# Kernel tuning notes

Measured on AMD Instinct MI355X. Metric: run time of the kernel, lower is better.

The kernel has to match this reference:

```python
import jax, jax.numpy as jnp
import numpy as np

EPS = 1e-12
B, DIN, T, DH = 32, 512, 4096, 500


def setup_inputs() -> dict:
    key = jax.random.key(0)
    k1, k2, k3 = jax.random.split(key, 3)
    x = jax.random.normal(k1, (B, DIN, T), dtype=jnp.float32)
    weight1 = jax.random.normal(k2, (DH, DIN), dtype=jnp.float32) * (1.0 / np.sqrt(DIN))
    weight2 = jax.random.normal(k3, (1, DH), dtype=jnp.float32) * (1.0 / np.sqrt(DH))
    return {"x": x, "weight1": weight1, "weight2": weight2, "dim": 2}


def reference(x, weight1, weight2, dim):
    # x: (B, din, T)
    h = jnp.swapaxes(x, 1, 2)                      # (B, T, din)
    a = jax.nn.relu(jnp.einsum('btd,hd->bth', h, weight1))  # (B, T, dh)
    scores = jnp.einsum('bth,oh->bto', a, weight2)           # (B, T, 1)
    attn = jax.nn.softmax(scores, axis=1)                    # softmax over time
    mean = jnp.einsum('bdt,bto->bdo', x, attn)               # (B, din, 1)
    variance = jnp.mean((x - mean) ** 2, axis=dim)           # (B, din) unweighted
    mean_s = jnp.squeeze(mean, axis=dim)                     # (B, din)
    mask = (variance <= EPS).astype(variance.dtype)
    variance = (1.0 - mask) * variance + mask * EPS
    stddev = jnp.sqrt(variance)
    return jnp.concatenate((mean_s, stddev), axis=-1)        # (B, 2*din)
```

## Files before the change

kernel.cpp:

```cpp
#include <hip/hip_runtime.h>
#include <hip/hip_bf16.h>

#define NB 32
#define DIN 512
#define TT 4096
#define DH 500
#define DHP 512
#define EPSV 1e-12f
#define BM 128
#define LDA 520
#define NTILES (TT / BM)
#define CHD 128
#define NCHK 4

typedef short short8 __attribute__((ext_vector_type(8)));
typedef float f32x16 __attribute__((ext_vector_type(16)));

__device__ inline unsigned short f2bf(float f) {
    unsigned int u = __builtin_bit_cast(unsigned int, f);
    unsigned int r = (u + 0x7fffu + ((u >> 16) & 1u)) >> 16;
    return (unsigned short)r;
}
__device__ inline float bf2f(unsigned short h) {
    unsigned int u = ((unsigned int)h) << 16;
    return __builtin_bit_cast(float, u);
}

__global__ void prep_kernel(const float* __restrict__ w1, const float* __restrict__ w2,
                            unsigned short* __restrict__ w1b, float* __restrict__ w2f) {
    int idx = blockIdx.x * blockDim.x + threadIdx.x;
    if (idx < DHP * DIN) {
        const int j    = idx & 7;
        const int lane = (idx >> 3) & 63;
        const int ks   = (idx >> 9) & 31;
        const int hb   = idx >> 14;
        const int h = hb * 32 + (lane & 31);
        const int d = ks * 16 + (lane >> 5) * 8 + j;
        float v = (h < DH) ? w1[h * DIN + d] : 0.f;
        w1b[idx] = f2bf(v);
        if (idx < DHP) w2f[idx] = (idx < DH) ? w2[idx] : 0.f;
    }
}

__launch_bounds__(512, 2)
__global__ void scores_fused(const float* __restrict__ x,
                             const unsigned short* __restrict__ w1b,
                             const float* __restrict__ w2f,
                             float* __restrict__ pm, float* __restrict__ pz,
                             float* __restrict__ pswx, float* __restrict__ psx,
                             float* __restrict__ psx2) {
    __shared__ unsigned short A_lds[BM][LDA];
    __shared__ float score_p[8][BM];
    __shared__ float w_lds[BM];
    __shared__ float red[4];

    const int tid = threadIdx.x;
    const int b  = blockIdx.x >> 5;
    const int t0 = (blockIdx.x & 31) * BM;

    const int tsub  = tid & 63;
    const int thalf = (tid >> 6) & 1;
    const int ts    = thalf * 64 + tsub;
    const int dg    = tid >> 7;
    const float* xb = x + (size_t)b * DIN * TT + t0 + ts;

    const int w = tid >> 6;
    const int lane = tid & 63;
    const int lane31 = lane & 31;
    const int khalf = lane >> 5;
    const int hrow0 = w * 64;
    const unsigned short* base0 = w1b + (size_t)w * 32768 + (size_t)lane * 8;
    const unsigned short* base1 = base0 + 16384;

    {
        float xr[32];
        #pragma unroll
        for (int j = 0; j < 32; ++j)
            xr[j] = xb[(size_t)(dg * 32 + j) * TT];
        #pragma unroll
        for (int oct = 0; oct < 4; ++oct) {
            short8 pk;
            #pragma unroll
            for (int j = 0; j < 8; ++j) pk[j] = (short)f2bf(xr[oct * 8 + j]);
            *reinterpret_cast<short8*>(&A_lds[ts][dg * 32 + oct * 8]) = pk;
        }
    }
    __syncthreads();

    f32x16 acc[2][4];
    #pragma unroll
    for (int p = 0; p < 2; ++p)
        #pragma unroll
        for (int tt = 0; tt < 4; ++tt)
            #pragma unroll
            for (int g = 0; g < 16; ++g) acc[p][tt][g] = 0.f;

    #pragma unroll
    for (int c = 0; c < NCHK; ++c) {
        float xr[32];
        if (c < NCHK - 1) {
            const int db = (c + 1) * CHD + dg * 32;
            #pragma unroll
            for (int j = 0; j < 32; ++j)
                xr[j] = xb[(size_t)(db + j) * TT];
        }
        __builtin_amdgcn_sched_barrier(0);

        #pragma unroll
        for (int ks = 0; ks < 8; ++ks) {
            const int k = c * 8 + ks;
            short8 a0 = *reinterpret_cast<const short8*>(base0 + k * 512);
            short8 a1 = *reinterpret_cast<const short8*>(base1 + k * 512);
            #pragma unroll
            for (int tt = 0; tt < 4; ++tt) {
                short8 bb = *reinterpret_cast<const short8*>(
                    &A_lds[tt * 32 + lane31][k * 16 + khalf * 8]);
                acc[0][tt] = __builtin_amdgcn_mfma_f32_32x32x16_bf16(a0, bb, acc[0][tt], 0, 0, 0);
                acc[1][tt] = __builtin_amdgcn_mfma_f32_32x32x16_bf16(a1, bb, acc[1][tt], 0, 0, 0);
            }
        }

        if (c < NCHK - 1) {
            const int db = (c + 1) * CHD + dg * 32;
            #pragma unroll
            for (int oct = 0; oct < 4; ++oct) {
                short8 pk;
                #pragma unroll
                for (int j = 0; j < 8; ++j) pk[j] = (short)f2bf(xr[oct * 8 + j]);
                *reinterpret_cast<short8*>(&A_lds[ts][db + oct * 8]) = pk;
            }
        }
        __syncthreads();
    }

    #pragma unroll
    for (int tt = 0; tt < 4; ++tt) {
        float s = 0.f;
        #pragma unroll
        for (int g = 0; g < 16; ++g) {
            const int rp = (g & 3) + 8 * (g >> 2) + 4 * khalf;
            s += fmaxf(acc[0][tt][g], 0.f) * w2f[hrow0 + rp]
               + fmaxf(acc[1][tt][g], 0.f) * w2f[hrow0 + 32 + rp];
        }
        s += __shfl_xor(s, 32, 64);
        if (khalf == 0) score_p[w][tt * 32 + lane31] = s;
    }
    __syncthreads();

    const int tl = tid & 127;
    float sv = 0.f;
    if (tid < BM) {
        #pragma unroll
        for (int ww = 0; ww < 8; ++ww) sv += score_p[ww][tl];
    }
    float m = (tid < BM) ? sv : -1e30f;
    #pragma unroll
    for (int k = 1; k <= 32; k <<= 1) m = fmaxf(m, __shfl_xor(m, k, 64));
    if (tid == 0) red[0] = m;
    if (tid == 64) red[1] = m;
    __syncthreads();
    const float mb = fmaxf(red[0], red[1]);
    float e = 0.f, Zp = 0.f;
    if (tid < BM) { e = __expf(sv - mb); Zp = e; }
    #pragma unroll
    for (int k = 1; k <= 32; k <<= 1) Zp += __shfl_xor(Zp, k, 64);
    if (tid == 0) red[2] = Zp;
    if (tid == 64) red[3] = Zp;
    if (tid < BM) w_lds[tl] = e;
    __syncthreads();
    if (tid == 0) { pm[blockIdx.x] = mb; pz[blockIdx.x] = red[2] + red[3]; }

    {
        const int d = tid;
        float sx = 0.f, sx2 = 0.f, swx = 0.f;
        #pragma unroll 8
        for (int t = 0; t < BM; ++t) {
            const float xv = bf2f(A_lds[t][d]);
            const float wv = w_lds[t];
            sx += xv; sx2 += xv * xv; swx += wv * xv;
        }
        const size_t o = (size_t)blockIdx.x * DHP + d;
        psx[o] = sx; psx2[o] = sx2; pswx[o] = swx;
    }
}

__global__ void combine_kernel(const float* __restrict__ pm, const float* __restrict__ pz,
                               const float* __restrict__ pswx, const float* __restrict__ psx,
                               const float* __restrict__ psx2, float* __restrict__ out) {
    __shared__ float sm[NTILES], sz[NTILES];
    const int b = blockIdx.x;
    const int tid = threadIdx.x;
    if (tid < NTILES) { sm[tid] = pm[b * NTILES + tid]; sz[tid] = pz[b * NTILES + tid]; }
    __syncthreads();

    float mg = -1e30f;
    #pragma unroll 8
    for (int i = 0; i < NTILES; ++i) mg = fmaxf(mg, sm[i]);
    float denom = 0.f;
    #pragma unroll 8
    for (int i = 0; i < NTILES; ++i) denom += sz[i] * __expf(sm[i] - mg);

    float num = 0.f, sx = 0.f, sx2 = 0.f;
    #pragma unroll 4
    for (int i = 0; i < NTILES; ++i) {
        const size_t o = ((size_t)(b * NTILES + i)) * DHP + tid;
        const float f = __expf(sm[i] - mg);
        num += f * pswx[o];
        sx  += psx[o];
        sx2 += psx2[o];
    }
    const float mean = num / denom;
    const float ex  = sx  * (1.f / TT);
    const float ex2 = sx2 * (1.f / TT);
    float var = ex2 - 2.f * mean * ex + mean * mean;
    if (var <= EPSV) var = EPSV;
    out[(size_t)b * 1024 + tid] = mean;
    out[(size_t)b * 1024 + 512 + tid] = sqrtf(var);
}

extern "C" void kernel_launch(void* const* d_in, const int* in_sizes, int n_in,
                              void* d_out, int out_size, void* d_ws, size_t ws_size,
                              hipStream_t stream) {
    const float* x  = (const float*)d_in[0];
    const float* w1 = (const float*)d_in[1];
    const float* w2 = (const float*)d_in[2];
    float* out = (float*)d_out;

    char* ws = (char*)d_ws;
    unsigned short* w1b = (unsigned short*)ws;
    float* w2f  = (float*)(ws + 524288);
    float* pm   = (float*)(ws + 526336);
    float* pz   = (float*)(ws + 530432);
    float* pswx = (float*)(ws + 534528);
    float* psx  = pswx + (size_t)NB * NTILES * DHP;
    float* psx2 = psx  + (size_t)NB * NTILES * DHP;

    prep_kernel<<<(DHP * DIN + 255) / 256, 256, 0, stream>>>(w1, w2, w1b, w2f);
    scores_fused<<<NB * NTILES, 512, 0, stream>>>(x, w1b, w2f, pm, pz, pswx, psx, psx2);
    combine_kernel<<<NB, 512, 0, stream>>>(pm, pz, pswx, psx, psx2, out);
}
```

Baseline: 129.2 us.

## Double-buffer weight fragments in registers, vectorize x loads, and vectorize the stats pass

Weight fragments for the next K chunk are now prefetched into a double-buffered register array ahead of the MFMA loop, so the MFMAs no longer wait on global loads issued inside the inner loop. The x tile is loaded as float4 along time with a new thread mapping, giving wider global loads and transposed bf16 packing into LDS. The per-column statistics pass reads short8 vectors from LDS and reduces across lanes with shuffles instead of scalar strided reads. The cost is many more VGPRs for the prefetched fragments, which may cause spills or lower occupancy under the 512x2 launch bounds.

```diff
diff --git a/kernel.cpp b/kernel.cpp
--- a/kernel.cpp
+++ b/kernel.cpp
@@ -12,9 +12,11 @@
 #define NTILES (TT / BM)
 #define CHD 128
 #define NCHK 4
+#define KSC 8
 
 typedef short short8 __attribute__((ext_vector_type(8)));
 typedef float f32x16 __attribute__((ext_vector_type(16)));
+typedef float f32x4 __attribute__((ext_vector_type(4)));
 
 __device__ inline unsigned short f2bf(float f) {
     unsigned int u = __builtin_bit_cast(unsigned int, f);
@@ -58,11 +60,9 @@
     const int b  = blockIdx.x >> 5;
     const int t0 = (blockIdx.x & 31) * BM;
 
-    const int tsub  = tid & 63;
-    const int thalf = (tid >> 6) & 1;
-    const int ts    = thalf * 64 + tsub;
-    const int dg    = tid >> 7;
-    const float* xb = x + (size_t)b * DIN * TT + t0 + ts;
+    const int q  = tid & 31;
+    const int dr = tid >> 5;
+    const float* xq = x + (size_t)b * DIN * TT + t0 + 4 * q;
 
     const int w = tid >> 6;
     const int lane = tid & 63;
@@ -72,62 +72,72 @@
     const unsigned short* base0 = w1b + (size_t)w * 32768 + (size_t)lane * 8;
     const unsigned short* base1 = base0 + 16384;
 
+    short8 a0p[2][KSC], a1p[2][KSC];
+    f32x16 acc[2][4];
+    #pragma unroll
+    for (int p = 0; p < 2; ++p)
+        #pragma unroll
+        for (int tt = 0; tt < 4; ++tt)
+            #pragma unroll
+            for (int g = 0; g < 16; ++g) acc[p][tt][g] = 0.f;
+
+    #pragma unroll
+    for (int j = 0; j < KSC; ++j) {
+        a0p[0][j] = *reinterpret_cast<const short8*>(base0 + j * 512);
+        a1p[0][j] = *reinterpret_cast<const short8*>(base1 + j * 512);
+    }
+    __builtin_amdgcn_sched_barrier(0);
     {
-        float xr[32];
-        #pragma unroll
-        for (int j = 0; j < 32; ++j)
-            xr[j] = xb[(size_t)(dg * 32 + j) * TT];
-        #pragma unroll
-        for (int oct = 0; oct < 4; ++oct) {
+        f32x4 xv[8];
+        #pragma unroll
+        for (int j = 0; j < 8; ++j)
+            xv[j] = *reinterpret_cast<const f32x4*>(xq + (size_t)(dr * 8 + j) * TT);
+        __builtin_amdgcn_sched_barrier(0);
+        #pragma unroll
+        for (int i = 0; i < 4; ++i) {
             short8 pk;
             #pragma unroll
-            for (int j = 0; j < 8; ++j) pk[j] = (short)f2bf(xr[oct * 8 + j]);
-            *reinterpret_cast<short8*>(&A_lds[ts][dg * 32 + oct * 8]) = pk;
-        }
-    }
-    __syncthreads();
-
-    f32x16 acc[2][4];
-    #pragma unroll
-    for (int p = 0; p < 2; ++p)
-        #pragma unroll
-        for (int tt = 0; tt < 4; ++tt)
-            #pragma unroll
-            for (int g = 0; g < 16; ++g) acc[p][tt][g] = 0.f;
+            for (int j = 0; j < 8; ++j) pk[j] = (short)f2bf(xv[j][i]);
+            *reinterpret_cast<short8*>(&A_lds[4 * q + i][dr * 8]) = pk;
+        }
+    }
+    __syncthreads();
 
     #pragma unroll
     for (int c = 0; c < NCHK; ++c) {
-        float xr[32];
-        if (c < NCHK - 1) {
-            const int db = (c + 1) * CHD + dg * 32;
-            #pragma unroll
-            for (int j = 0; j < 32; ++j)
-                xr[j] = xb[(size_t)(db + j) * TT];
+        const int cb = c & 1;
+        f32x4 xv[8];
+        if (c + 1 < NCHK) {
+            #pragma unroll
+            for (int j = 0; j < KSC; ++j) {
+                a0p[cb ^ 1][j] = *reinterpret_cast<const short8*>(base0 + ((c + 1) * KSC + j) * 512);
+                a1p[cb ^ 1][j] = *reinterpret_cast<const short8*>(base1 + ((c + 1) * KSC + j) * 512);
+            }
+            __builtin_amdgcn_sched_barrier(0);
+            #pragma unroll
+            for (int j = 0; j < 8; ++j)
+                xv[j] = *reinterpret_cast<const f32x4*>(xq + (size_t)((c + 1) * CHD + dr * 8 + j) * TT);
         }
         __builtin_amdgcn_sched_barrier(0);
-
-        #pragma unroll
-        for (int ks = 0; ks < 8; ++ks) {
-            const int k = c * 8 + ks;
-            short8 a0 = *reinterpret_cast<const short8*>(base0 + k * 512);
-            short8 a1 = *reinterpret_cast<const short8*>(base1 + k * 512);
+        #pragma unroll
+        for (int ks = 0; ks < KSC; ++ks) {
+            const int k = c * KSC + ks;
             #pragma unroll
             for (int tt = 0; tt < 4; ++tt) {
                 short8 bb = *reinterpret_cast<const short8*>(
                     &A_lds[tt * 32 + lane31][k * 16 + khalf * 8]);
-                acc[0][tt] = __builtin_amdgcn_mfma_f32_32x32x16_bf16(a0, bb, acc[0][tt], 0, 0, 0);
-                acc[1][tt] = __builtin_amdgcn_mfma_f32_32x32x16_bf16(a1, bb, acc[1][tt], 0, 0, 0);
-            }
-        }
-
-        if (c < NCHK - 1) {
-            const int db = (c + 1) * CHD + dg * 32;
-            #pragma unroll
-            for (int oct = 0; oct < 4; ++oct) {
+                acc[0][tt] = __builtin_amdgcn_mfma_f32_32x32x16_bf16(a0p[cb][ks], bb, acc[0][tt], 0, 0, 0);
+                acc[1][tt] = __builtin_amdgcn_mfma_f32_32x32x16_bf16(a1p[cb][ks], bb, acc[1][tt], 0, 0, 0);
+            }
+        }
+        __builtin_amdgcn_sched_barrier(0);
+        if (c + 1 < NCHK) {
+            #pragma unroll
+            for (int i = 0; i < 4; ++i) {
                 short8 pk;
                 #pragma unroll
-                for (int j = 0; j < 8; ++j) pk[j] = (short)f2bf(xr[oct * 8 + j]);
-                *reinterpret_cast<short8*>(&A_lds[ts][db + oct * 8]) = pk;
+                for (int j = 0; j < 8; ++j) pk[j] = (short)f2bf(xv[j][i]);
+                *reinterpret_cast<short8*>(&A_lds[4 * q + i][(c + 1) * CHD + dr * 8]) = pk;
             }
         }
         __syncthreads();
@@ -171,16 +181,40 @@
     if (tid == 0) { pm[blockIdx.x] = mb; pz[blockIdx.x] = red[2] + red[3]; }
 
     {
-        const int d = tid;
-        float sx = 0.f, sx2 = 0.f, swx = 0.f;
-        #pragma unroll 8
-        for (int t = 0; t < BM; ++t) {
-            const float xv = bf2f(A_lds[t][d]);
+        const int o = lane & 7;
+        const int g = lane >> 3;
+        float sx8[8], sx28[8], swx8[8];
+        #pragma unroll
+        for (int e2 = 0; e2 < 8; ++e2) { sx8[e2] = 0.f; sx28[e2] = 0.f; swx8[e2] = 0.f; }
+        #pragma unroll
+        for (int t5 = 0; t5 < 16; ++t5) {
+            const int t = g * 16 + t5;
+            short8 xv8 = *reinterpret_cast<const short8*>(&A_lds[t][w * 64 + o * 8]);
             const float wv = w_lds[t];
-            sx += xv; sx2 += xv * xv; swx += wv * xv;
-        }
-        const size_t o = (size_t)blockIdx.x * DHP + d;
-        psx[o] = sx; psx2[o] = sx2; pswx[o] = swx;
+            #pragma unroll
+            for (int e2 = 0; e2 < 8; ++e2) {
+                const float f = bf2f((unsigned short)xv8[e2]);
+                sx8[e2] += f; sx28[e2] += f * f; swx8[e2] += wv * f;
+            }
+        }
+        #pragma unroll
+        for (int mk = 8; mk <= 32; mk <<= 1) {
+            #pragma unroll
+            for (int e2 = 0; e2 < 8; ++e2) {
+                sx8[e2]  += __shfl_xor(sx8[e2],  mk, 64);
+                sx28[e2] += __shfl_xor(sx28[e2], mk, 64);
+                swx8[e2] += __shfl_xor(swx8[e2], mk, 64);
+            }
+        }
+        if (g == 0) {
+            const size_t ob = (size_t)blockIdx.x * DHP + w * 64 + o * 8;
+            #pragma unroll
+            for (int e2 = 0; e2 < 8; ++e2) {
+                psx[ob + e2]  = sx8[e2];
+                psx2[ob + e2] = sx28[e2];
+                pswx[ob + e2] = swx8[e2];
+            }
+        }
     }
 }
 
```

New measurement: 190.7 us. +47.6%, slower.
